# Performance work log

Measured on AMD Instinct MI355X. Metric: run time of the kernel, lower is better.

Reference implementation:

```python
import jax, jax.numpy as jnp
import numpy as np

E = 8      # N_experts (hard-coded in module)
K = 2      # top-k (hard-coded in module)


def setup_inputs() -> dict:
    key = jax.random.key(0)
    ks = jax.random.split(key, 8)
    B, T, d = 4, 2048, 1024
    h = 4 * d // E  # 512, per Expert hidden_dim = 4*d//N_experts
    s = 0.02
    X = jax.random.normal(ks[0], (B, T, d), jnp.float32)
    routing_W = jax.random.normal(ks[1], (E, d), jnp.float32) * s  # Linear(d,E,bias=False).weight
    expert_bias = jnp.zeros((E,), jnp.float32)
    sW1 = jax.random.normal(ks[2], (d, h), jnp.float32) * s
    sb1 = jnp.zeros((h,), jnp.float32)
    sW2 = jax.random.normal(ks[3], (h, d), jnp.float32) * s
    sb2 = jnp.zeros((d,), jnp.float32)
    rW1 = jax.random.normal(ks[4], (E, d, h), jnp.float32) * s
    rb1 = jnp.zeros((E, h), jnp.float32)
    rW2 = jax.random.normal(ks[5], (E, h, d), jnp.float32) * s
    rb2 = jnp.zeros((E, d), jnp.float32)
    return dict(X=X, routing_W=routing_W, expert_bias=expert_bias,
                sW1=sW1, sb1=sb1, sW2=sW2, sb2=sb2,
                rW1=rW1, rb1=rb1, rW2=rW2, rb2=rb2)


def reference(X, routing_W, expert_bias, sW1, sb1, sW2, sb2, rW1, rb1, rW2, rb2):
    B, T, d = X.shape
    # Shared expert MLP: Linear -> SiLU -> Linear
    shared = jax.nn.silu(X @ sW1 + sb1) @ sW2 + sb2  # [B,T,d]

    # Routing (layer_idx in {3,4,5} path): logits -> sqrt(softplus) -> top-2
    logits = jnp.einsum('btd,ed->bte', X, routing_W) + expert_bias  # [B,T,E]
    activation = jnp.sqrt(jax.nn.softplus(logits))
    top_vals, top_idx = jax.lax.top_k(activation, K)  # [B,T,K]

    # Per-token combine weights over experts: sum_k top_vals[k] * onehot(top_idx[k])
    combine = jnp.sum(jax.nn.one_hot(top_idx, E, dtype=X.dtype) * top_vals[..., None],
                      axis=-2)  # [B,T,E]

    # Dense all-expert compute (equivalent to masked gather + per-expert MLP +
    # scatter-add combine in the original; unrouted experts get weight 0).
    Xf = X.reshape(-1, d)          # [N,d], N = B*T
    cf = combine.reshape(-1, E)    # [N,E]
    hdn = jax.nn.silu(jnp.einsum('nd,edh->enh', Xf, rW1) + rb1[:, None, :])  # [E,N,h]
    y = jnp.einsum('enh,ehd->end', hdn, rW2) + rb2[:, None, :]               # [E,N,d]
    routed = jnp.einsum('ne,end->nd', cf, y).reshape(B, T, d)

    return shared + routed
```

## Files before the change

### kernel.cpp

```cpp
#include <hip/hip_runtime.h>
#include <hip/hip_bf16.h>
#include <stdint.h>

#define NTOK 8192
#define DDIM 1024
#define HDIM 512

typedef __attribute__((ext_vector_type(8))) __bf16 bf16x8;
typedef __attribute__((ext_vector_type(4))) float f32x4;
typedef __attribute__((ext_vector_type(4))) uint32_t u32x4;
typedef __attribute__((ext_vector_type(2))) uint32_t u32x2;

__device__ __forceinline__ void gload16(const void* g, void* lds) {
  __builtin_amdgcn_global_load_lds(
      (const __attribute__((address_space(1))) void*)g,
      (__attribute__((address_space(3))) void*)lds,
      16, 0, 0);
}


__global__ __launch_bounds__(256)
void convert_route_kernel(const float* __restrict__ X, const float* __restrict__ rW,
                          const float* __restrict__ ebias,
                          __hip_bfloat16* __restrict__ Xb,
                          int* __restrict__ top_e, float* __restrict__ top_w) {
  int wid = threadIdx.x >> 6, lane = threadIdx.x & 63;
  int tok = blockIdx.x * 4 + wid;
  const float4* xr = (const float4*)(X + (size_t)tok * DDIM);
  u32x2* xb = (u32x2*)(Xb + (size_t)tok * DDIM);
  float acc[8];
  #pragma unroll
  for (int e = 0; e < 8; e++) acc[e] = 0.f;
  #pragma unroll
  for (int c = 0; c < 4; c++) {
    int j = c * 64 + lane;
    float4 x = xr[j];
    union { __hip_bfloat16 h[4]; u32x2 u; } cv;
    cv.h[0] = __float2bfloat16(x.x); cv.h[1] = __float2bfloat16(x.y);
    cv.h[2] = __float2bfloat16(x.z); cv.h[3] = __float2bfloat16(x.w);
    xb[j] = cv.u;
    #pragma unroll
    for (int e = 0; e < 8; e++) {
      float4 w = ((const float4*)(rW + (size_t)e * DDIM))[j];
      acc[e] += x.x * w.x + x.y * w.y + x.z * w.z + x.w * w.w;
    }
  }
  #pragma unroll
  for (int m = 1; m < 64; m <<= 1)
    #pragma unroll
    for (int e = 0; e < 8; e++) acc[e] += __shfl_xor(acc[e], m, 64);
  if (lane == 0) {
    float act[8];
    #pragma unroll
    for (int e = 0; e < 8; e++) {
      float x = acc[e] + ebias[e];
      float sp = (x > 15.f) ? x : log1pf(expf(x));
      act[e] = sqrtf(sp);
    }
    int e1 = 0; float v1 = act[0];
    #pragma unroll
    for (int e = 1; e < 8; e++) if (act[e] > v1) { v1 = act[e]; e1 = e; }
    int e2 = -1; float v2 = -1.f;
    #pragma unroll
    for (int e = 0; e < 8; e++) if (e != e1 && act[e] > v2) { v2 = act[e]; e2 = e; }
    top_e[tok * 2] = e1; top_e[tok * 2 + 1] = e2;
    top_w[tok * 2] = v1; top_w[tok * 2 + 1] = v2;
  }
}

__global__ void convert_w_kernel(const float* __restrict__ in, __hip_bfloat16* __restrict__ out,
                                 int K, int Nn) {
  __shared__ float tile[32][33];
  const float* src = in + (size_t)blockIdx.z * K * Nn;
  __hip_bfloat16* dst = out + (size_t)blockIdx.z * K * Nn;
  int n0 = blockIdx.x * 32, k0 = blockIdx.y * 32;
  int c = threadIdx.x & 31, r = threadIdx.x >> 5;
  #pragma unroll
  for (int i = 0; i < 4; i++)
    tile[r + i * 8][c] = src[(size_t)(k0 + r + i * 8) * Nn + n0 + c];
  __syncthreads();
  #pragma unroll
  for (int i = 0; i < 4; i++)
    dst[(size_t)(n0 + r + i * 8) * K + k0 + c] = __float2bfloat16(tile[c][r + i * 8]);
}


__global__ void hist_kernel(const int* __restrict__ top_e, int* __restrict__ chunkHist) {
  __shared__ int h[8];
  if (threadIdx.x < 8) h[threadIdx.x] = 0;
  __syncthreads();
  int a = blockIdx.x * 256 + threadIdx.x;
  atomicAdd(&h[top_e[a]], 1);
  __syncthreads();
  if (threadIdx.x < 8) chunkHist[blockIdx.x * 8 + threadIdx.x] = h[threadIdx.x];
}

__global__ void scan_kernel(const int* __restrict__ chunkHist, int* __restrict__ chunkBase,
                            int* __restrict__ counts, int* __restrict__ offs) {
  int e = threadIdx.x;
  if (e < 8) {
    int run = 0;
    for (int b = 0; b < 64; b++) { chunkBase[b * 8 + e] = run; run += chunkHist[b * 8 + e]; }
    counts[e] = run;
  }
  __syncthreads();
  if (e == 0) {
    int s = 0;
    for (int i = 0; i < 8; i++) { offs[i] = s; s += counts[i]; }
    offs[8] = s;
  }
  __syncthreads();
  if (e < 8) {
    int base = offs[e];
    for (int b = 0; b < 64; b++) chunkBase[b * 8 + e] += base;
  }
}

__global__ void scatter_kernel(const int* __restrict__ top_e, const float* __restrict__ top_w,
                               const int* __restrict__ chunkBase,
                               int* __restrict__ list, float* __restrict__ wlist,
                               int* __restrict__ inv) {
  __shared__ int lcnt[8];
  if (threadIdx.x < 8) lcnt[threadIdx.x] = 0;
  __syncthreads();
  int a = blockIdx.x * 256 + threadIdx.x;
  int e = top_e[a];
  int p = atomicAdd(&lcnt[e], 1);
  int pos = chunkBase[blockIdx.x * 8 + e] + p;
  list[pos] = a >> 1;
  wlist[pos] = top_w[a];
  inv[a] = pos;
}


__global__ __launch_bounds__(256)
void combine_kernel(const int* __restrict__ inv, const __hip_bfloat16* __restrict__ ybuf,
                    float* __restrict__ out) {
  int tok = blockIdx.x;
  int c = threadIdx.x * 4;
  int p0 = inv[tok * 2], p1 = inv[tok * 2 + 1];
  size_t o = (size_t)tok * DDIM + c;
  float4 v = *(const float4*)(out + o);
  union { u32x2 u; __hip_bfloat16 h[4]; } y0, y1;
  y0.u = *(const u32x2*)(ybuf + (size_t)p0 * DDIM + c);
  y1.u = *(const u32x2*)(ybuf + (size_t)p1 * DDIM + c);
  v.x += __bfloat162float(y0.h[0]) + __bfloat162float(y1.h[0]);
  v.y += __bfloat162float(y0.h[1]) + __bfloat162float(y1.h[1]);
  v.z += __bfloat162float(y0.h[2]) + __bfloat162float(y1.h[2]);
  v.w += __bfloat162float(y0.h[3]) + __bfloat162float(y1.h[3]);
  *(float4*)(out + o) = v;
}


template<int MODE>
__global__ __launch_bounds__(256, 2)
void gemm_kernel(const __hip_bfloat16* __restrict__ Abase,
                 const __hip_bfloat16* __restrict__ Ws,
                 const __hip_bfloat16* __restrict__ Wr,
                 const float* __restrict__ bs,
                 const float* __restrict__ br,
                 __hip_bfloat16* __restrict__ Hout,
                 float* __restrict__ Oout,
                 __hip_bfloat16* __restrict__ Ybuf,
                 const int* __restrict__ counts,
                 const int* __restrict__ offs,
                 const int* __restrict__ list,
                 const float* __restrict__ wlist) {
  constexpr int K  = (MODE == 1) ? 1024 : 512;
  constexpr int NN = (MODE == 1) ? 512 : 1024;
  constexpr int LDB = K * 2;

  __shared__ __hip_bfloat16 Abuf[128 * 32];
  __shared__ __hip_bfloat16 Bbuf[128 * 32];
  __shared__ int tokens[128];

  int bid = blockIdx.x;
  int e = 0, mt, nt;
  bool rb = false;
  if (MODE == 1) {
    if (bid < 256) { mt = bid >> 2; nt = bid & 3; }
    else { rb = true; int q = bid - 256; e = q >> 8; q &= 255; mt = q >> 2; nt = q & 3; }
  } else if (MODE == 2) { mt = bid >> 3; nt = bid & 7; }
  else { rb = true; e = bid >> 9; int q = bid & 511; mt = q >> 3; nt = q & 7; }
  int m0 = mt * 128;
  int cnt = 128;
  if (rb) {
    int ce = counts[e];
    if (m0 >= ce) return;
    cnt = (ce - m0 < 128) ? (ce - m0) : 128;
  }

  const __hip_bfloat16* W = rb ? (Wr + (size_t)e * NN * K) : Ws;
  const float* bias = rb ? (br + e * NN) : bs;

  int tid = threadIdx.x, wid = tid >> 6, lane = tid & 63;
  if (MODE == 1) {
    if (tid < 128)
      tokens[tid] = rb ? ((tid < cnt) ? list[offs[e] + m0 + tid] : 0) : (m0 + tid);
    __syncthreads();
  }
  int arow0 = (MODE == 2) ? m0 : ((MODE == 3) ? (NTOK + offs[e] + m0) : 0);

  const char* aSrc[2];
  const char* bSrc[2];
  int ldsOff[2];
  #pragma unroll
  for (int c = 0; c < 2; c++) {
    int s = c * 4096 + wid * 1024 + lane * 16;
    int row = s >> 6;
    int chunk = (s >> 4) & 3;
    int sc = chunk ^ (row & 3);
    long ar = (MODE == 1) ? (long)tokens[row] : (long)(arow0 + row);
    aSrc[c] = (const char*)Abase + (size_t)ar * LDB + sc * 16;
    bSrc[c] = (const char*)W + (size_t)(nt * 128 + row) * LDB + sc * 16;
    ldsOff[c] = c * 4096 + wid * 1024;
  }

  int wm = wid >> 1, wn = wid & 1;
  int aoff[4], boff[4];
  #pragma unroll
  for (int m = 0; m < 4; m++) {
    int row = wm * 64 + m * 16 + (lane & 15);
    aoff[m] = row * 64 + (((lane >> 4) ^ (row & 3)) << 4);
  }
  #pragma unroll
  for (int n = 0; n < 4; n++) {
    int row = wn * 64 + n * 16 + (lane & 15);
    boff[n] = row * 64 + (((lane >> 4) ^ (row & 3)) << 4);
  }

  f32x4 zero = {0.f, 0.f, 0.f, 0.f};
  f32x4 acc[4][4];
  #pragma unroll
  for (int m = 0; m < 4; m++)
    #pragma unroll
    for (int n = 0; n < 4; n++) acc[m][n] = zero;

  char* ldsA = (char*)&Abuf[0];
  char* ldsB = (char*)&Bbuf[0];

  for (int kt = 0; kt < K / 32; ++kt) {
    __syncthreads();
    #pragma unroll
    for (int c = 0; c < 2; c++) gload16(aSrc[c] + (size_t)kt * 64, ldsA + ldsOff[c]);
    #pragma unroll
    for (int c = 0; c < 2; c++) gload16(bSrc[c] + (size_t)kt * 64, ldsB + ldsOff[c]);
    __syncthreads();
    bf16x8 a[4], b[4];
    #pragma unroll
    for (int m = 0; m < 4; m++) a[m] = *(const bf16x8*)(ldsA + aoff[m]);
    #pragma unroll
    for (int n = 0; n < 4; n++) b[n] = *(const bf16x8*)(ldsB + boff[n]);
    #pragma unroll
    for (int m = 0; m < 4; m++)
      #pragma unroll
      for (int n = 0; n < 4; n++)
        acc[m][n] = __builtin_amdgcn_mfma_f32_16x16x32_bf16(a[m], b[n], acc[m][n], 0, 0, 0);
  }

  int colBase = nt * 128 + wn * 64;
  if (MODE == 1) {
    size_t hrow0 = rb ? (size_t)(NTOK + offs[e] + m0) : (size_t)m0;
    #pragma unroll
    for (int m = 0; m < 4; m++) {
      #pragma unroll
      for (int r = 0; r < 4; r++) {
        int rl = wm * 64 + m * 16 + ((lane >> 4) << 2) + r;
        if (rl < cnt) {
          #pragma unroll
          for (int n = 0; n < 4; n++) {
            int col = colBase + n * 16 + (lane & 15);
            float v = acc[m][n][r] + bias[col];
            v = v / (1.f + __expf(-v));
            Hout[(hrow0 + rl) * HDIM + col] = __float2bfloat16(v);
          }
        }
      }
    }
  } else if (MODE == 2) {
    #pragma unroll
    for (int m = 0; m < 4; m++) {
      #pragma unroll
      for (int r = 0; r < 4; r++) {
        int rl = wm * 64 + m * 16 + ((lane >> 4) << 2) + r;
        size_t orow = (size_t)(m0 + rl);
        #pragma unroll
        for (int n = 0; n < 4; n++) {
          int col = colBase + n * 16 + (lane & 15);
          Oout[orow * DDIM + col] = acc[m][n][r] + bias[col];
        }
      }
    }
  } else {
    #pragma unroll
    for (int m = 0; m < 4; m++) {
      #pragma unroll
      for (int r = 0; r < 4; r++) {
        int rl = wm * 64 + m * 16 + ((lane >> 4) << 2) + r;
        if (rl < cnt) {
          int pos = offs[e] + m0 + rl;
          float w = wlist[pos];
          #pragma unroll
          for (int n = 0; n < 4; n++) {
            int col = colBase + n * 16 + (lane & 15);
            Ybuf[(size_t)pos * DDIM + col] = __float2bfloat16(w * (acc[m][n][r] + bias[col]));
          }
        }
      }
    }
  }
}


extern "C" void kernel_launch(void* const* d_in, const int* in_sizes, int n_in,
                              void* d_out, int out_size, void* d_ws, size_t ws_size,
                              hipStream_t stream) {
  const float* X   = (const float*)d_in[0];
  const float* rWt = (const float*)d_in[1];
  const float* eb  = (const float*)d_in[2];
  const float* sW1 = (const float*)d_in[3];
  const float* sb1 = (const float*)d_in[4];
  const float* sW2 = (const float*)d_in[5];
  const float* sb2 = (const float*)d_in[6];
  const float* rW1 = (const float*)d_in[7];
  const float* rb1 = (const float*)d_in[8];
  const float* rW2 = (const float*)d_in[9];
  const float* rb2 = (const float*)d_in[10];
  float* out = (float*)d_out;

  char* ws = (char*)d_ws;
  size_t off = 0;
  auto alloc = [&](size_t bytes) {
    char* p = ws + off;
    off += (bytes + 255) & ~(size_t)255;
    return p;
  };
  char* region0 = alloc((size_t)16384 * DDIM * 2);
  __hip_bfloat16* Xb   = (__hip_bfloat16*)region0;
  __hip_bfloat16* sW1t = (__hip_bfloat16*)(region0 + (size_t)NTOK * DDIM * 2);
  __hip_bfloat16* rW1t = (__hip_bfloat16*)(region0 + (size_t)NTOK * DDIM * 2
                                                   + (size_t)HDIM * DDIM * 2);
  __hip_bfloat16* Ybuf = (__hip_bfloat16*)region0;

  __hip_bfloat16* sW2t = (__hip_bfloat16*)alloc((size_t)DDIM * HDIM * 2);
  __hip_bfloat16* rW2t = (__hip_bfloat16*)alloc((size_t)8 * DDIM * HDIM * 2);
  __hip_bfloat16* Hbuf = (__hip_bfloat16*)alloc((size_t)(NTOK + 2 * NTOK) * HDIM * 2);
  alloc(131072);
  int* counts    = (int*)alloc(64);
  int* offsA     = (int*)alloc(64);
  int* top_e     = (int*)alloc((size_t)NTOK * 2 * 4);
  float* top_w   = (float*)alloc((size_t)NTOK * 2 * 4);
  int* list      = (int*)alloc((size_t)NTOK * 2 * 4);
  float* wlist   = (float*)alloc((size_t)NTOK * 2 * 4);
  int* inv       = (int*)alloc((size_t)NTOK * 2 * 4);
  int* chunkHist = (int*)alloc(64 * 8 * 4);
  int* chunkBase = (int*)alloc(64 * 8 * 4);

  convert_route_kernel<<<2048, 256, 0, stream>>>(X, rWt, eb, Xb, top_e, top_w);
  convert_w_kernel<<<dim3(16, 32, 1), 256, 0, stream>>>(sW1, sW1t, 1024, 512);
  convert_w_kernel<<<dim3(32, 16, 1), 256, 0, stream>>>(sW2, sW2t, 512, 1024);
  convert_w_kernel<<<dim3(16, 32, 8), 256, 0, stream>>>(rW1, rW1t, 1024, 512);
  convert_w_kernel<<<dim3(32, 16, 8), 256, 0, stream>>>(rW2, rW2t, 512, 1024);
  hist_kernel<<<64, 256, 0, stream>>>(top_e, chunkHist);
  scan_kernel<<<1, 64, 0, stream>>>(chunkHist, chunkBase, counts, offsA);
  scatter_kernel<<<64, 256, 0, stream>>>(top_e, top_w, chunkBase, list, wlist, inv);
  gemm_kernel<1><<<256 + 8 * 64 * 4, 256, 0, stream>>>(Xb, sW1t, rW1t, sb1, rb1, Hbuf, out,
                                                       nullptr, counts, offsA, list, wlist);
  gemm_kernel<2><<<64 * 8, 256, 0, stream>>>(Hbuf, sW2t, rW2t, sb2, rb2, nullptr, out,
                                             nullptr, counts, offsA, list, wlist);
  gemm_kernel<3><<<8 * 64 * 8, 256, 0, stream>>>(Hbuf, sW2t, rW2t, sb2, rb2, nullptr, out,
                                                 Ybuf, counts, offsA, list, wlist);
  combine_kernel<<<NTOK, 256, 0, stream>>>(inv, Ybuf, out);
}
```

Baseline: 288.7 us.

## Compact routed GEMM tile grid, merge GEMM2 launches, swizzle blocks across XCDs

Adds a per-expert tile-prefix array so routed GEMM blocks map densely onto real work. This replaces the old grid sized for the worst case, where many blocks exited immediately. The shared and routed second GEMMs are merged into one launch (MODE 23), the weight conversions are fused into two launches, and block indices are remapped so consecutive tiles spread across the 8 XCDs. Launch bounds are raised to 4 blocks per CU, which may increase register pressure or spilling.

New measurement: 264.1 us. 8.5% less time.

```diff
diff --git a/kernel.cpp b/kernel.cpp
--- a/kernel.cpp
+++ b/kernel.cpp
@@ -68,11 +68,13 @@
   }
 }
 
-__global__ void convert_w_kernel(const float* __restrict__ in, __hip_bfloat16* __restrict__ out,
+__global__ void convert_w_kernel(const float* __restrict__ sIn, const float* __restrict__ rIn,
+                                 __hip_bfloat16* __restrict__ sOut, __hip_bfloat16* __restrict__ rOut,
                                  int K, int Nn) {
   __shared__ float tile[32][33];
-  const float* src = in + (size_t)blockIdx.z * K * Nn;
-  __hip_bfloat16* dst = out + (size_t)blockIdx.z * K * Nn;
+  int z = blockIdx.z;
+  const float* src = (z == 0) ? sIn : rIn + (size_t)(z - 1) * K * Nn;
+  __hip_bfloat16* dst = (z == 0) ? sOut : rOut + (size_t)(z - 1) * K * Nn;
   int n0 = blockIdx.x * 32, k0 = blockIdx.y * 32;
   int c = threadIdx.x & 31, r = threadIdx.x >> 5;
   #pragma unroll
@@ -96,7 +98,8 @@
 }
 
 __global__ void scan_kernel(const int* __restrict__ chunkHist, int* __restrict__ chunkBase,
-                            int* __restrict__ counts, int* __restrict__ offs) {
+                            int* __restrict__ counts, int* __restrict__ offs,
+                            int* __restrict__ tiles) {
   int e = threadIdx.x;
   if (e < 8) {
     int run = 0;
@@ -108,6 +111,9 @@
     int s = 0;
     for (int i = 0; i < 8; i++) { offs[i] = s; s += counts[i]; }
     offs[8] = s;
+    int tb = 0;
+    for (int i = 0; i < 8; i++) { tiles[i] = tb; tb += (counts[i] + 127) >> 7; }
+    tiles[8] = tb;
   }
   __syncthreads();
   if (e < 8) {
@@ -153,7 +159,7 @@
 
 
 template<int MODE>
-__global__ __launch_bounds__(256, 2)
+__global__ __launch_bounds__(256, 4)
 void gemm_kernel(const __hip_bfloat16* __restrict__ Abase,
                  const __hip_bfloat16* __restrict__ Ws,
                  const __hip_bfloat16* __restrict__ Wr,
@@ -164,29 +170,36 @@
                  __hip_bfloat16* __restrict__ Ybuf,
                  const int* __restrict__ counts,
                  const int* __restrict__ offs,
+                 const int* __restrict__ tiles,
                  const int* __restrict__ list,
                  const float* __restrict__ wlist) {
-  constexpr int K  = (MODE == 1) ? 1024 : 512;
-  constexpr int NN = (MODE == 1) ? 512 : 1024;
+  constexpr int K   = (MODE == 1) ? 1024 : 512;
+  constexpr int NN  = (MODE == 1) ? 512 : 1024;
   constexpr int LDB = K * 2;
+  constexpr int SH  = (MODE == 1) ? 256 : 512;
+  constexpr int LNT = (MODE == 1) ? 2 : 3;
 
   __shared__ __hip_bfloat16 Abuf[128 * 32];
   __shared__ __hip_bfloat16 Bbuf[128 * 32];
   __shared__ int tokens[128];
 
-  int bid = blockIdx.x;
+  int l = ((blockIdx.x & 7) * (gridDim.x >> 3)) + (blockIdx.x >> 3);
+
   int e = 0, mt, nt;
   bool rb = false;
-  if (MODE == 1) {
-    if (bid < 256) { mt = bid >> 2; nt = bid & 3; }
-    else { rb = true; int q = bid - 256; e = q >> 8; q &= 255; mt = q >> 2; nt = q & 3; }
-  } else if (MODE == 2) { mt = bid >> 3; nt = bid & 7; }
-  else { rb = true; e = bid >> 9; int q = bid & 511; mt = q >> 3; nt = q & 7; }
+  if (l < SH) { mt = l >> LNT; nt = l & ((1 << LNT) - 1); }
+  else {
+    rb = true;
+    int rq = l - SH;
+    int rt = rq >> LNT; nt = rq & ((1 << LNT) - 1);
+    if (rt >= tiles[8]) return;
+    while (e < 7 && rt >= tiles[e + 1]) ++e;
+    mt = rt - tiles[e];
+  }
   int m0 = mt * 128;
   int cnt = 128;
   if (rb) {
     int ce = counts[e];
-    if (m0 >= ce) return;
     cnt = (ce - m0 < 128) ? (ce - m0) : 128;
   }
 
@@ -199,7 +212,7 @@
       tokens[tid] = rb ? ((tid < cnt) ? list[offs[e] + m0 + tid] : 0) : (m0 + tid);
     __syncthreads();
   }
-  int arow0 = (MODE == 2) ? m0 : ((MODE == 3) ? (NTOK + offs[e] + m0) : 0);
+  int arow0 = rb ? (NTOK + offs[e] + m0) : m0;
 
   const char* aSrc[2];
   const char* bSrc[2];
@@ -277,7 +290,7 @@
         }
       }
     }
-  } else if (MODE == 2) {
+  } else if (!rb) {
     #pragma unroll
     for (int m = 0; m < 4; m++) {
       #pragma unroll
@@ -348,6 +361,7 @@
   alloc(131072);
   int* counts    = (int*)alloc(64);
   int* offsA     = (int*)alloc(64);
+  int* tiles     = (int*)alloc(64);
   int* top_e     = (int*)alloc((size_t)NTOK * 2 * 4);
   float* top_w   = (float*)alloc((size_t)NTOK * 2 * 4);
   int* list      = (int*)alloc((size_t)NTOK * 2 * 4);
@@ -357,18 +371,14 @@
   int* chunkBase = (int*)alloc(64 * 8 * 4);
 
   convert_route_kernel<<<2048, 256, 0, stream>>>(X, rWt, eb, Xb, top_e, top_w);
-  convert_w_kernel<<<dim3(16, 32, 1), 256, 0, stream>>>(sW1, sW1t, 1024, 512);
-  convert_w_kernel<<<dim3(32, 16, 1), 256, 0, stream>>>(sW2, sW2t, 512, 1024);
-  convert_w_kernel<<<dim3(16, 32, 8), 256, 0, stream>>>(rW1, rW1t, 1024, 512);
-  convert_w_kernel<<<dim3(32, 16, 8), 256, 0, stream>>>(rW2, rW2t, 512, 1024);
+  convert_w_kernel<<<dim3(16, 32, 9), 256, 0, stream>>>(sW1, rW1, sW1t, rW1t, 1024, 512);
+  convert_w_kernel<<<dim3(32, 16, 9), 256, 0, stream>>>(sW2, rW2, sW2t, rW2t, 512, 1024);
   hist_kernel<<<64, 256, 0, stream>>>(top_e, chunkHist);
-  scan_kernel<<<1, 64, 0, stream>>>(chunkHist, chunkBase, counts, offsA);
+  scan_kernel<<<1, 64, 0, stream>>>(chunkHist, chunkBase, counts, offsA, tiles);
   scatter_kernel<<<64, 256, 0, stream>>>(top_e, top_w, chunkBase, list, wlist, inv);
-  gemm_kernel<1><<<256 + 8 * 64 * 4, 256, 0, stream>>>(Xb, sW1t, rW1t, sb1, rb1, Hbuf, out,
-                                                       nullptr, counts, offsA, list, wlist);
-  gemm_kernel<2><<<64 * 8, 256, 0, stream>>>(Hbuf, sW2t, rW2t, sb2, rb2, nullptr, out,
-                                             nullptr, counts, offsA, list, wlist);
-  gemm_kernel<3><<<8 * 64 * 8, 256, 0, stream>>>(Hbuf, sW2t, rW2t, sb2, rb2, nullptr, out,
-                                                 Ybuf, counts, offsA, list, wlist);
+  gemm_kernel<1><<<256 + 4 * 136, 256, 0, stream>>>(Xb, sW1t, rW1t, sb1, rb1, Hbuf, out,
+                                                    nullptr, counts, offsA, tiles, list, wlist);
+  gemm_kernel<23><<<512 + 8 * 136, 256, 0, stream>>>(Hbuf, sW2t, rW2t, sb2, rb2, nullptr, out,
+                                                     Ybuf, counts, offsA, tiles, list, wlist);
   combine_kernel<<<NTOK, 256, 0, stream>>>(inv, Ybuf, out);
 }
```
